# Optimization experiments

Measured on AMD Instinct MI355X. Metric: run time of the kernel, lower is better.

Reference implementation:

```python
import jax, jax.numpy as jnp
import numpy as np

B, K, R = 16, 256, 256          # batch, text length, encoder dim (r_out_size)
CONV_OUT = 8                    # l_conv_out_size
SW_C = 16                       # l_swish_c_out_size
SW_W = 16                       # l_swish_w_out_size
KS = 3                          # l_conv_kernel_size
T_MAX = 1000                    # torch.clamp(pred_mel_len, max=1000) -> static frame dim
BN_EPS = 1e-5
LN_EPS = 1e-5


def _layer_norm(x, g, b):
    mu = jnp.mean(x, -1, keepdims=True)
    var = jnp.var(x, -1, keepdims=True)
    return (x - mu) * jax.lax.rsqrt(var + LN_EPS) * g + b


def _conv_block(V, w, b, bn_g, bn_b, ln_g, ln_b):
    # ConvBlock: Conv1d(SAME) -> eval BatchNorm (running mean 0 / var 1) -> SiLU -> LayerNorm
    x = jax.lax.conv_general_dilated(V, w, (1,), "SAME",
                                     dimension_numbers=("NWC", "WIO", "NWC")) + b
    x = x * (bn_g / jnp.sqrt(1.0 + BN_EPS)) + bn_b
    x = jax.nn.silu(x)
    return _layer_norm(x, ln_g, ln_b)


def _swish_block(S, E, V8, w1, b1, w2, b2):
    # SwishBlock: Linear(concat([S,E,V8], -1)) -> SiLU -> Linear -> SiLU,
    # without materializing the [B,T,K,CONV_OUT+2] concat (split the first matmul).
    base = V8 @ w1[2:] + b1                                           # [B,K,H]
    h = jax.nn.silu(S[..., None] * w1[0] + E[..., None] * w1[1] + base[:, None])  # [B,T,K,H]
    return jax.nn.silu(h @ w2 + b2)


def setup_inputs():
    key = jax.random.key(0)
    ks = jax.random.split(key, 20)
    f32 = jnp.float32

    inp = {}
    # durations ~ U[0,10): per-utterance sum ~1280 >> T_MAX, so every length clamps to T_MAX
    inp["dur"] = jax.random.uniform(ks[0], (B, K), dtype=f32) * 10.0
    inp["V"] = jax.random.normal(ks[1], (B, K, R), dtype=f32)
    inp["pos_text"] = jnp.tile(jnp.arange(K, dtype=jnp.int32)[None], (B, 1))
    inp["text_mask"] = jnp.zeros((B, K), dtype=bool)

    def n(k, shape, s):
        return jax.random.normal(k, shape, dtype=f32) * s

    for tag, i in (("c", 2), ("w", 6)):
        inp[f"conv_{tag}_w"] = n(ks[i], (KS, R, CONV_OUT), 0.05)
        inp[f"conv_{tag}_b"] = jnp.zeros((CONV_OUT,), f32)
        inp[f"bn_{tag}_g"] = jnp.ones((CONV_OUT,), f32)
        inp[f"bn_{tag}_b"] = jnp.zeros((CONV_OUT,), f32)
        inp[f"ln_{tag}_g"] = jnp.ones((CONV_OUT,), f32)
        inp[f"ln_{tag}_b"] = jnp.zeros((CONV_OUT,), f32)
    inp["swc_w1"] = n(ks[10], (CONV_OUT + 2, SW_C), 0.3)
    inp["swc_b1"] = jnp.zeros((SW_C,), f32)
    inp["swc_w2"] = n(ks[11], (SW_C, SW_C), 0.3)
    inp["swc_b2"] = jnp.zeros((SW_C,), f32)
    inp["sww_w1"] = n(ks[12], (CONV_OUT + 2, SW_W), 0.3)
    inp["sww_b1"] = jnp.zeros((SW_W,), f32)
    inp["sww_w2"] = n(ks[13], (SW_W, SW_W), 0.3)
    inp["sww_b2"] = jnp.zeros((SW_W,), f32)
    inp["proj_w_w"] = n(ks[14], (SW_W, 1), 0.3)
    inp["proj_w_b"] = jnp.zeros((1,), f32)
    inp["lin_e_w"] = n(ks[15], (SW_C, R), 0.1)
    inp["lin_e_b"] = jnp.zeros((R,), f32)
    inp["ln_o_g"] = jnp.ones((R,), f32)
    inp["ln_o_b"] = jnp.zeros((R,), f32)
    return inp


def reference(dur, V, pos_text, text_mask,
              conv_c_w, conv_c_b, bn_c_g, bn_c_b, ln_c_g, ln_c_b,
              conv_w_w, conv_w_b, bn_w_g, bn_w_b, ln_w_g, ln_w_b,
              swc_w1, swc_b1, swc_w2, swc_b2,
              sww_w1, sww_b1, sww_w2, sww_b2,
              proj_w_w, proj_w_b, lin_e_w, lin_e_b, ln_o_g, ln_o_b):
    pred_mel_len = jnp.minimum(jnp.round(dur.sum(-1)), T_MAX).astype(jnp.int32)  # [B]
    pred_mel_mask = jnp.arange(T_MAX, dtype=jnp.int32)[None, :] >= pred_mel_len[:, None]  # [B,T]
    tm = text_mask[:, None, :]       # [B,1,K]
    mm = pred_mel_mask[:, :, None]   # [B,T,1]
    attn_mask = tm | mm              # [B,T,K]

    e_k = jnp.cumsum(dur, axis=1)    # token end boundaries   [B,K]
    s_k = e_k - dur                  # token start boundaries [B,K]
    t = jnp.arange(1, T_MAX + 1, dtype=dur.dtype)[None, :, None]   # frame index [1,T,1]
    S = jnp.where(attn_mask, 0.0, t - s_k[:, None, :])             # [B,T,K]
    E = jnp.where(attn_mask, 0.0, e_k[:, None, :] - t)             # [B,T,K]

    Vw = _conv_block(V, conv_w_w, conv_w_b, bn_w_g, bn_w_b, ln_w_g, ln_w_b)
    Wh = _swish_block(S, E, Vw, sww_w1, sww_b1, sww_w2, sww_b2)    # [B,T,K,SW_W]
    logits = jnp.squeeze(Wh @ proj_w_w, -1) + proj_w_b[0]          # [B,T,K]
    logits = jnp.where(tm, -jnp.inf, logits)
    W = jax.nn.softmax(logits, axis=2)
    W = jnp.where(mm, 0.0, W)

    Vc = _conv_block(V, conv_c_w, conv_c_b, bn_c_g, bn_c_b, ln_c_g, ln_c_b)
    C = _swish_block(S, E, Vc, swc_w1, swc_b1, swc_w2, swc_b2)     # [B,T,K,SW_C]

    agg = jnp.einsum("btk,btkp->btp", W, C)                        # [B,T,SW_C]
    up = jnp.matmul(W, V) + (agg @ lin_e_w + lin_e_b)              # [B,T,R]
    up = _layer_norm(up, ln_o_g, ln_o_b)
    up = jnp.where(pred_mel_mask[..., None], 0.0, up)
    return up, pred_mel_mask, pred_mel_len, W
```

## Files before the change

kernel.cpp:

```cpp
#include <hip/hip_runtime.h>
#include <cstddef>

constexpr int Bn = 16, Kn = 256, Rn = 256, Tn = 1000, C8 = 8, SW = 16;
constexpr size_t UP_SZ    = (size_t)Bn * Tn * Rn;
constexpr size_t MASK_OFF = UP_SZ;
constexpr size_t LEN_OFF  = MASK_OFF + (size_t)Bn * Tn;
constexpr size_t W_OFF    = LEN_OFF + Bn;

using half4_t = __attribute__((ext_vector_type(4))) _Float16;
using f32x4_t = __attribute__((ext_vector_type(4))) float;
using uint2_t = __attribute__((ext_vector_type(2))) unsigned int;

__device__ __forceinline__ float fast_rcp(float x) { return __builtin_amdgcn_rcpf(x); }
__device__ __forceinline__ float fast_exp2(float x) { return __builtin_amdgcn_exp2f(x); }
constexpr float LOG2E = 1.44269504088896340736f;
__device__ __forceinline__ float silu_f(float x) {
    return x * fast_rcp(1.f + fast_exp2(-LOG2E * x));
}

__device__ __forceinline__ void split4(const float x0, const float x1,
                                       const float x2, const float x3,
                                       half4_t& hi, half4_t& lo)
{
    const auto h01 = __builtin_amdgcn_cvt_pkrtz(x0, x1);
    const auto h23 = __builtin_amdgcn_cvt_pkrtz(x2, x3);
    uint2_t uh; uh.x = __builtin_bit_cast(unsigned int, h01);
    uh.y = __builtin_bit_cast(unsigned int, h23);
    hi = __builtin_bit_cast(half4_t, uh);
    const auto l01 = __builtin_amdgcn_cvt_pkrtz(x0 - (float)h01.x, x1 - (float)h01.y);
    const auto l23 = __builtin_amdgcn_cvt_pkrtz(x2 - (float)h23.x, x3 - (float)h23.y);
    uint2_t ul; ul.x = __builtin_bit_cast(unsigned int, l01);
    ul.y = __builtin_bit_cast(unsigned int, l23);
    lo = __builtin_bit_cast(half4_t, ul);
}

__global__ __launch_bounds__(256) void conv_partial_kernel(
    const float* __restrict__ V,
    const float* __restrict__ wW, const float* __restrict__ wC,
    float* __restrict__ part)
{
    const int rc = blockIdx.x, b = blockIdx.y, k = threadIdx.x;
    constexpr int RPAD = 33;
    __shared__ float vt[258 * RPAD];
    if (k < 16) {
        const int row = (k < 8) ? 0 : 257;
        const int j = (k & 7) * 4;
        vt[row * RPAD + j] = 0.f; vt[row * RPAD + j + 1] = 0.f;
        vt[row * RPAD + j + 2] = 0.f; vt[row * RPAD + j + 3] = 0.f;
    }
    const float* vsrc = V + ((size_t)(b * Kn + k)) * Rn + rc * 32;
#pragma unroll
    for (int j = 0; j < 8; j++) {
        const float4 qv = *(const float4*)(vsrc + j * 4);
        float* dst = &vt[(k + 1) * RPAD + j * 4];
        dst[0] = qv.x; dst[1] = qv.y; dst[2] = qv.z; dst[3] = qv.w;
    }
    __syncthreads();

    float aw[C8], ac[C8];
#pragma unroll
    for (int c = 0; c < C8; c++) { aw[c] = 0.f; ac[c] = 0.f; }
    for (int dk = 0; dk < 3; dk++) {
        const float* wp = wW + (size_t)(dk * Rn + rc * 32) * C8;
        const float* cp = wC + (size_t)(dk * Rn + rc * 32) * C8;
        const float* vrow = &vt[(k + dk) * RPAD];
#pragma unroll 4
        for (int r = 0; r < 32; r++) {
            const float v = vrow[r];
#pragma unroll
            for (int c = 0; c < C8; c++) {
                aw[c] = fmaf(v, wp[r * C8 + c], aw[c]);
                ac[c] = fmaf(v, cp[r * C8 + c], ac[c]);
            }
        }
    }
    float* dst = part + ((size_t)(b * 8 + rc) * Kn + k) * 16;
    *(float4*)(dst + 0)  = make_float4(aw[0], aw[1], aw[2], aw[3]);
    *(float4*)(dst + 4)  = make_float4(aw[4], aw[5], aw[6], aw[7]);
    *(float4*)(dst + 8)  = make_float4(ac[0], ac[1], ac[2], ac[3]);
    *(float4*)(dst + 12) = make_float4(ac[4], ac[5], ac[6], ac[7]);
}

__device__ __forceinline__ void conv_post(
    const float* acc, const float* cb, const float* bng, const float* bnb,
    const float* lng, const float* lnb, const float* w1, const float* b1,
    float* __restrict__ dst)
{
    const float bnscale = rsqrtf(1.f + 1e-5f);
    float x[C8];
    float mu = 0.f;
#pragma unroll
    for (int c = 0; c < C8; c++) {
        float v = (acc[c] + cb[c]) * (bng[c] * bnscale) + bnb[c];
        v = silu_f(v);
        x[c] = v; mu += v;
    }
    mu *= (1.f / C8);
    float var = 0.f;
#pragma unroll
    for (int c = 0; c < C8; c++) { float dd = x[c] - mu; var += dd * dd; }
    var *= (1.f / C8);
    const float rs = rsqrtf(var + 1e-5f);
    float y[C8];
#pragma unroll
    for (int c = 0; c < C8; c++) y[c] = (x[c] - mu) * rs * lng[c] + lnb[c];
#pragma unroll
    for (int c2 = 0; c2 < SW; c2++) {
        float a = b1[c2];
#pragma unroll
        for (int p = 0; p < C8; p++) a = fmaf(y[p], w1[(2 + p) * SW + c2], a);
        dst[c2] = a;
    }
}

__global__ __launch_bounds__(256) void conv_scan_finish_kernel(
    const float* __restrict__ dur,
    const float* __restrict__ part,
    const unsigned char* __restrict__ tmask_g,
    const float* __restrict__ bW, const float* __restrict__ bngW, const float* __restrict__ bnbW,
    const float* __restrict__ lngW, const float* __restrict__ lnbW,
    const float* __restrict__ bC, const float* __restrict__ bngC, const float* __restrict__ bnbC,
    const float* __restrict__ lngC, const float* __restrict__ lnbC,
    const float* __restrict__ sww_w1, const float* __restrict__ sww_b1,
    const float* __restrict__ swc_w1, const float* __restrict__ swc_b1,
    float* __restrict__ alpha_ws, float* __restrict__ ab_ws,
    int* __restrict__ len_ws, float* __restrict__ out)
{
    const int b = blockIdx.x, k = threadIdx.x;
    __shared__ float sc[Kn];
    const float d = dur[b * Kn + k];
    sc[k] = d;
    __syncthreads();
    for (int off = 1; off < Kn; off <<= 1) {
        float v = (k >= off) ? sc[k - off] : 0.f;
        __syncthreads();
        sc[k] += v;
        __syncthreads();
    }
    const float ek = sc[k];
    const float sk = ek - d;
    const float total = sc[Kn - 1];
    int len = (int)rintf(total);
    if (len > Tn) len = Tn;
    if (k == 0) { len_ws[b] = len; out[LEN_OFF + b] = (float)len; }
    for (int t = k; t < Tn; t += 256)
        out[MASK_OFF + (size_t)b * Tn + t] = (t >= len) ? 1.f : 0.f;
    if (b == 0 && k < 16) {
        alpha_ws[k]      = sww_w1[k] - sww_w1[SW + k];
        alpha_ws[16 + k] = swc_w1[k] - swc_w1[SW + k];
    }

    float aw[C8], ac[C8];
#pragma unroll
    for (int c = 0; c < C8; c++) { aw[c] = 0.f; ac[c] = 0.f; }
#pragma unroll 2
    for (int rc = 0; rc < 8; rc++) {
        const float4* p = (const float4*)(part + ((size_t)(b * 8 + rc) * Kn + k) * 16);
        const float4 q0 = p[0], q1 = p[1], q2 = p[2], q3 = p[3];
        aw[0] += q0.x; aw[1] += q0.y; aw[2] += q0.z; aw[3] += q0.w;
        aw[4] += q1.x; aw[5] += q1.y; aw[6] += q1.z; aw[7] += q1.w;
        ac[0] += q2.x; ac[1] += q2.y; ac[2] += q2.z; ac[3] += q2.w;
        ac[4] += q3.x; ac[5] += q3.y; ac[6] += q3.z; ac[7] += q3.w;
    }
    float basew[SW], basec[SW];
    conv_post(aw, bW, bngW, bnbW, lngW, lnbW, sww_w1, sww_b1, basew);
    conv_post(ac, bC, bngC, bnbC, lngC, lnbC, swc_w1, swc_b1, basec);

    const bool msk = tmask_g[b * Kn + k] != 0;
    float* dst = ab_ws + ((size_t)(b * Kn) + k) * 32;
#pragma unroll
    for (int c = 0; c < SW; c++) {
        const float w0w = sww_w1[c], w1w_ = sww_w1[SW + c];
        const float w0c = swc_w1[c], w1c_ = swc_w1[SW + c];
        dst[c]      = msk ? basew[c] : fmaf(ek, w1w_, fmaf(-sk, w0w, basew[c]));
        dst[16 + c] = msk ? basec[c] : fmaf(ek, w1c_, fmaf(-sk, w0c, basec[c]));
    }
}

__global__ __launch_bounds__(256) void logits_kernel(
    const unsigned char* __restrict__ tm, const int* __restrict__ len_ws,
    const float* __restrict__ alpha_ws, const float* __restrict__ ab_ws,
    const float* __restrict__ sww_w2, const float* __restrict__ sww_b2,
    const float* __restrict__ proj_w, const float* __restrict__ proj_b,
    const float* __restrict__ swc_w2, const float* __restrict__ swc_b2,
    float* __restrict__ agg_ws, float* __restrict__ out)
{
    const int t0 = blockIdx.x * 4, b = blockIdx.y, tid = threadIdx.x;
    const int lane = tid & 63, w = tid >> 6, q = lane >> 4, m = lane & 15;
    const int len = len_ws[b];

    __shared__ __align__(16) unsigned int hA[256 * 10];
    __shared__ __align__(16) unsigned int hB[256 * 10];
    __shared__ __align__(16) unsigned int hC[256 * 10];
    __shared__ float red[8];
    __shared__ __align__(16) float aggw[2][4][16];

    float bw[16], bc[16];
    {
        const float4* bp = (const float4*)(ab_ws + (((size_t)b * Kn) + tid) * 32);
#pragma unroll
        for (int i = 0; i < 4; i++) {
            const float4 v = bp[i];
            bw[4*i] = v.x; bw[4*i+1] = v.y; bw[4*i+2] = v.z; bw[4*i+3] = v.w;
        }
#pragma unroll
        for (int i = 0; i < 4; i++) {
            const float4 v = bp[4 + i];
            bc[4*i] = v.x; bc[4*i+1] = v.y; bc[4*i+2] = v.z; bc[4*i+3] = v.w;
        }
    }
    const float mk = (tm[b * Kn + tid] != 0) ? 0.f : 1.f;

    half4_t AWhi, AWlo, ACf;
    float pj[4], b2wv[4], b2cv[4], mb[4];
#pragma unroll
    for (int i = 0; i < 4; i++) {
        const int c = 4 * q + i;
        const float vw = sww_w2[c * SW + m];
        const _Float16 hi = (_Float16)vw;
        AWhi[i] = hi;
        AWlo[i] = (_Float16)(vw - (float)hi);
        ACf[i]  = (_Float16)(swc_w2[c * SW + m]);
        pj[i]   = proj_w[c];
        b2wv[i] = sww_b2[c];
        b2cv[i] = swc_b2[c];
        mb[i]   = (tm[b * Kn + 64 * w + 16 * i + m] != 0) ? -INFINITY : 0.f;
    }
    const float pb = proj_b[0];

    int pend = -1, pendpar = 0;

    for (int ti = 0; ti < 4; ti++) {
        const int t = t0 + ti;
        float* __restrict__ W_out = out + W_OFF + ((size_t)b * Tn + t) * Kn;
        if (t >= len) { W_out[tid] = 0.f; continue; }
        const float u = (float)(t + 1);
        const float umk = u * mk;

#pragma unroll
        for (int p = 0; p < 8; p++) {
            const float x0 = fmaf(umk, alpha_ws[2*p],   bw[2*p]);
            const float x1 = fmaf(umk, alpha_ws[2*p+1], bw[2*p+1]);
            const float h0 = silu_f(x0), h1 = silu_f(x1);
            const auto hp = __builtin_amdgcn_cvt_pkrtz(h0, h1);
            hA[tid * 10 + p] = __builtin_bit_cast(unsigned int, hp);
            const float l0 = h0 - (float)hp.x, l1 = h1 - (float)hp.y;
            hB[tid * 10 + p] = __builtin_bit_cast(unsigned int,
                                __builtin_amdgcn_cvt_pkrtz(l0, l1));
            const float y0 = fmaf(umk, alpha_ws[16 + 2*p],   bc[2*p]);
            const float y1 = fmaf(umk, alpha_ws[16 + 2*p+1], bc[2*p+1]);
            hC[tid * 10 + p] = __builtin_bit_cast(unsigned int,
                                __builtin_amdgcn_cvt_pkrtz(silu_f(y0), silu_f(y1)));
        }

        f32x4_t o[4];
#pragma unroll
        for (int j = 0; j < 4; j++) {
            const int row = 64 * w + 16 * j + m;
            const uint2_t rh = *(const uint2_t*)&hA[row * 10 + 2 * q];
            const uint2_t rl = *(const uint2_t*)&hB[row * 10 + 2 * q];
            const half4_t bh = __builtin_bit_cast(half4_t, rh);
            const half4_t bl = __builtin_bit_cast(half4_t, rl);
            f32x4_t acc = {0.f, 0.f, 0.f, 0.f};
            acc = __builtin_amdgcn_mfma_f32_16x16x16f16(AWlo, bh, acc, 0, 0, 0);
            acc = __builtin_amdgcn_mfma_f32_16x16x16f16(AWhi, bl, acc, 0, 0, 0);
            acc = __builtin_amdgcn_mfma_f32_16x16x16f16(AWhi, bh, acc, 0, 0, 0);
            o[j] = acc;
        }

        float lg[4];
#pragma unroll
        for (int j = 0; j < 4; j++) {
            float s = silu_f(o[j][0] + b2wv[0]) * pj[0];
            s = fmaf(silu_f(o[j][1] + b2wv[1]), pj[1], s);
            s = fmaf(silu_f(o[j][2] + b2wv[2]), pj[2], s);
            s = fmaf(silu_f(o[j][3] + b2wv[3]), pj[3], s);
            s += __shfl_xor(s, 16, 64);
            s += __shfl_xor(s, 32, 64);
            lg[j] = s + pb + mb[j];
        }

        float mx = fmaxf(fmaxf(lg[0], lg[1]), fmaxf(lg[2], lg[3]));
#pragma unroll
        for (int off = 1; off <= 8; off <<= 1) mx = fmaxf(mx, __shfl_xor(mx, off, 64));
        if (lane == 0) red[w] = mx;
        __syncthreads();
        if (pend >= 0) {
            if (tid < 16)
                agg_ws[((size_t)b * Tn + pend) * 16 + tid] =
                    aggw[pendpar][0][tid] + aggw[pendpar][1][tid] +
                    aggw[pendpar][2][tid] + aggw[pendpar][3][tid];
            pend = -1;
        }
        const float M = fmaxf(fmaxf(red[0], red[1]), fmaxf(red[2], red[3]));
        float pex[4];
#pragma unroll
        for (int j = 0; j < 4; j++) pex[j] = fast_exp2(LOG2E * (lg[j] - M));
        float ssum = (pex[0] + pex[1]) + (pex[2] + pex[3]);
#pragma unroll
        for (int off = 1; off <= 8; off <<= 1) ssum += __shfl_xor(ssum, off, 64);
        if (lane == 0) red[4 + w] = ssum;
        __syncthreads();
        const float inv = fast_rcp(red[4] + red[5] + red[6] + red[7]);
        float wgt[4];
#pragma unroll
        for (int j = 0; j < 4; j++) wgt[j] = pex[j] * inv;
        if (q == 0) {
#pragma unroll
            for (int j = 0; j < 4; j++) W_out[64 * w + 16 * j + m] = wgt[j];
        }

        f32x4_t ap = {0.f, 0.f, 0.f, 0.f};
#pragma unroll
        for (int j = 0; j < 4; j++) {
            const int row = 64 * w + 16 * j + m;
            const uint2_t rc2 = *(const uint2_t*)&hC[row * 10 + 2 * q];
            f32x4_t zz = {0.f, 0.f, 0.f, 0.f};
            const f32x4_t oc = __builtin_amdgcn_mfma_f32_16x16x16f16(
                ACf, __builtin_bit_cast(half4_t, rc2), zz, 0, 0, 0);
#pragma unroll
            for (int i = 0; i < 4; i++)
                ap[i] = fmaf(silu_f(oc[i] + b2cv[i]), wgt[j], ap[i]);
        }
#pragma unroll
        for (int off = 1; off <= 8; off <<= 1) {
            ap[0] += __shfl_xor(ap[0], off, 64);
            ap[1] += __shfl_xor(ap[1], off, 64);
            ap[2] += __shfl_xor(ap[2], off, 64);
            ap[3] += __shfl_xor(ap[3], off, 64);
        }
        if (m == 0)
            *(float4*)&aggw[ti & 1][w][4 * q] = make_float4(ap[0], ap[1], ap[2], ap[3]);
        pend = t; pendpar = ti & 1;
    }
    if (pend >= 0) {
        __syncthreads();
        if (tid < 16)
            agg_ws[((size_t)b * Tn + pend) * 16 + tid] =
                aggw[pendpar][0][tid] + aggw[pendpar][1][tid] +
                aggw[pendpar][2][tid] + aggw[pendpar][3][tid];
    }
}

__global__ __launch_bounds__(256) void matvec_mfma_kernel(
    const float* __restrict__ Wg, const float* __restrict__ V,
    float* __restrict__ out)
{
    const int tb = blockIdx.x, rq = blockIdx.y, b = blockIdx.z;
    const int t0 = tb * 32, r0 = rq * 64;
    const int tid = threadIdx.x;
    const int lane = tid & 63, w = tid >> 6, q = lane >> 4, m = lane & 15;
    __shared__ float4 Wl[32 * 64];

    const float4* Wg4 = (const float4*)Wg;
#pragma unroll
    for (int ch = 0; ch < 8; ch++) {
        const int idx = ch * 256 + tid;
        const int row = idx >> 6, sl = idx & 63;
        const int t = t0 + row;
        const float4 v = (t < Tn) ? Wg4[((size_t)b * Tn + t) * 64 + sl]
                                  : make_float4(0.f, 0.f, 0.f, 0.f);
        Wl[row * 64 + (sl ^ (row & 7))] = v;
    }
    __syncthreads();

    const int tt = w & 1;
    const int rp = w >> 1;
    const int wrow = tt * 16 + m;
    const int rcol = r0 + rp * 32 + m;
    const float* Vb = V + (size_t)b * Kn * Rn;

    f32x4_t acc0 = {0.f, 0.f, 0.f, 0.f};
    f32x4_t acc1 = {0.f, 0.f, 0.f, 0.f};

#pragma unroll
    for (int ks = 0; ks < 16; ks++) {
        const float4 wv = Wl[wrow * 64 + ((ks * 4 + q) ^ (wrow & 7))];
        half4_t Ahi, Alo;
        split4(wv.x, wv.y, wv.z, wv.w, Ahi, Alo);

        const float* vp = Vb + (size_t)(ks * 16 + 4 * q) * Rn;
        const float b00 = vp[rcol],          b01 = vp[Rn + rcol];
        const float b02 = vp[2 * Rn + rcol], b03 = vp[3 * Rn + rcol];
        const float b10 = vp[rcol + 16],          b11 = vp[Rn + rcol + 16];
        const float b12 = vp[2 * Rn + rcol + 16], b13 = vp[3 * Rn + rcol + 16];
        half4_t Bh0, Bl0, Bh1, Bl1;
        split4(b00, b01, b02, b03, Bh0, Bl0);
        split4(b10, b11, b12, b13, Bh1, Bl1);

        acc0 = __builtin_amdgcn_mfma_f32_16x16x16f16(Alo, Bh0, acc0, 0, 0, 0);
        acc0 = __builtin_amdgcn_mfma_f32_16x16x16f16(Ahi, Bl0, acc0, 0, 0, 0);
        acc0 = __builtin_amdgcn_mfma_f32_16x16x16f16(Ahi, Bh0, acc0, 0, 0, 0);
        acc1 = __builtin_amdgcn_mfma_f32_16x16x16f16(Alo, Bh1, acc1, 0, 0, 0);
        acc1 = __builtin_amdgcn_mfma_f32_16x16x16f16(Ahi, Bl1, acc1, 0, 0, 0);
        acc1 = __builtin_amdgcn_mfma_f32_16x16x16f16(Ahi, Bh1, acc1, 0, 0, 0);
    }

#pragma unroll
    for (int i = 0; i < 4; i++) {
        const int t = t0 + tt * 16 + 4 * q + i;
        if (t < Tn) {
            float* rowp = out + ((size_t)b * Tn + t) * Rn + rcol;
            rowp[0]  = acc0[i];
            rowp[16] = acc1[i];
        }
    }
}

__global__ __launch_bounds__(256) void ln_kernel(
    const float* __restrict__ agg_ws, const int* __restrict__ len_ws,
    const float* __restrict__ lin_e_w, const float* __restrict__ lin_e_b,
    const float* __restrict__ ln_o_g, const float* __restrict__ ln_o_b,
    float* __restrict__ out)
{
    const int b = blockIdx.y, tid = threadIdx.x;
    const int sub = tid >> 6, lane = tid & 63;
    const int t = blockIdx.x * 4 + sub;
    const int r0 = lane * 4;
    float* __restrict__ row = out + ((size_t)b * Tn + t) * Rn;
    const int len = len_ws[b];
    if (t >= len) {
        *(float4*)(row + r0) = make_float4(0.f, 0.f, 0.f, 0.f);
        return;
    }

    float4 acc = *(const float4*)(row + r0);
    {
        const float4 be = *(const float4*)(lin_e_b + r0);
        acc.x += be.x; acc.y += be.y; acc.z += be.z; acc.w += be.w;
    }
    const float* aggp = agg_ws + ((size_t)b * Tn + t) * 16;
#pragma unroll
    for (int p = 0; p < 16; p++) {
        const float a = aggp[p];
        const float4 l = *(const float4*)(lin_e_w + p * Rn + r0);
        acc.x = fmaf(a, l.x, acc.x); acc.y = fmaf(a, l.y, acc.y);
        acc.z = fmaf(a, l.z, acc.z); acc.w = fmaf(a, l.w, acc.w);
    }

    float s = (acc.x + acc.y) + (acc.z + acc.w);
#pragma unroll
    for (int off = 1; off <= 32; off <<= 1) s += __shfl_xor(s, off, 64);
    const float mu = s * (1.f / Rn);
    const float d0 = acc.x - mu, d1 = acc.y - mu, d2 = acc.z - mu, d3 = acc.w - mu;
    float vr = d0 * d0 + d1 * d1 + d2 * d2 + d3 * d3;
#pragma unroll
    for (int off = 1; off <= 32; off <<= 1) vr += __shfl_xor(vr, off, 64);
    const float rs = rsqrtf(vr * (1.f / Rn) + 1e-5f);

    const float4 g = *(const float4*)(ln_o_g + r0);
    const float4 bb = *(const float4*)(ln_o_b + r0);
    float4 res;
    res.x = d0 * rs * g.x + bb.x;
    res.y = d1 * rs * g.y + bb.y;
    res.z = d2 * rs * g.z + bb.z;
    res.w = d3 * rs * g.w + bb.w;
    *(float4*)(row + r0) = res;
}

extern "C" void kernel_launch(void* const* d_in, const int* in_sizes, int n_in,
                              void* d_out, int out_size, void* d_ws, size_t ws_size,
                              hipStream_t stream)
{
    const float* dur       = (const float*)d_in[0];
    const float* V         = (const float*)d_in[1];
    const unsigned char* text_mask = (const unsigned char*)d_in[3];
    const float* conv_c_w  = (const float*)d_in[4];
    const float* conv_c_b  = (const float*)d_in[5];
    const float* bn_c_g    = (const float*)d_in[6];
    const float* bn_c_b    = (const float*)d_in[7];
    const float* ln_c_g    = (const float*)d_in[8];
    const float* ln_c_b    = (const float*)d_in[9];
    const float* conv_w_w  = (const float*)d_in[10];
    const float* conv_w_b  = (const float*)d_in[11];
    const float* bn_w_g    = (const float*)d_in[12];
    const float* bn_w_b    = (const float*)d_in[13];
    const float* ln_w_g    = (const float*)d_in[14];
    const float* ln_w_b    = (const float*)d_in[15];
    const float* swc_w1    = (const float*)d_in[16];
    const float* swc_b1    = (const float*)d_in[17];
    const float* swc_w2    = (const float*)d_in[18];
    const float* swc_b2    = (const float*)d_in[19];
    const float* sww_w1    = (const float*)d_in[20];
    const float* sww_b1    = (const float*)d_in[21];
    const float* sww_w2    = (const float*)d_in[22];
    const float* sww_b2    = (const float*)d_in[23];
    const float* proj_w_w  = (const float*)d_in[24];
    const float* proj_w_b  = (const float*)d_in[25];
    const float* lin_e_w   = (const float*)d_in[26];
    const float* lin_e_b   = (const float*)d_in[27];
    const float* ln_o_g    = (const float*)d_in[28];
    const float* ln_o_b    = (const float*)d_in[29];

    float* out = (float*)d_out;
    float* wsf = (float*)d_ws;
    int*   len_ws   = (int*)wsf;
    float* alpha_ws = wsf + 64;
    float* ab_ws    = wsf + 128;
    float* scratch  = ab_ws + 131072;
    float* part     = scratch;
    float* agg_ws   = scratch;

    conv_partial_kernel<<<dim3(8, Bn), dim3(256), 0, stream>>>(V, conv_w_w, conv_c_w, part);
    conv_scan_finish_kernel<<<dim3(Bn), dim3(256), 0, stream>>>(
        dur, part, text_mask,
        conv_w_b, bn_w_g, bn_w_b, ln_w_g, ln_w_b,
        conv_c_b, bn_c_g, bn_c_b, ln_c_g, ln_c_b,
        sww_w1, sww_b1, swc_w1, swc_b1,
        alpha_ws, ab_ws, len_ws, out);
    logits_kernel<<<dim3(Tn / 4, Bn), dim3(256), 0, stream>>>(
        text_mask, len_ws, alpha_ws, ab_ws,
        sww_w2, sww_b2, proj_w_w, proj_w_b,
        swc_w2, swc_b2,
        agg_ws, out);
    matvec_mfma_kernel<<<dim3((Tn + 31) / 32, 4, Bn), dim3(256), 0, stream>>>(
        out + W_OFF, V, out);
    ln_kernel<<<dim3(Tn / 4, Bn), dim3(256), 0, stream>>>(
        agg_ws, len_ws, lin_e_w, lin_e_b, ln_o_g, ln_o_b, out);
}
```

Measured before the change: 160.5 us.

## Fuse logits, W·V matvec and output layernorm into one kernel

```diff
diff --git a/kernel.cpp b/kernel.cpp
--- a/kernel.cpp
+++ b/kernel.cpp
@@ -177,23 +177,28 @@
     }
 }
 
-__global__ __launch_bounds__(256) void logits_kernel(
+__global__ __launch_bounds__(256) void fused_kernel(
     const unsigned char* __restrict__ tm, const int* __restrict__ len_ws,
     const float* __restrict__ alpha_ws, const float* __restrict__ ab_ws,
     const float* __restrict__ sww_w2, const float* __restrict__ sww_b2,
     const float* __restrict__ proj_w, const float* __restrict__ proj_b,
     const float* __restrict__ swc_w2, const float* __restrict__ swc_b2,
-    float* __restrict__ agg_ws, float* __restrict__ out)
-{
-    const int t0 = blockIdx.x * 4, b = blockIdx.y, tid = threadIdx.x;
+    const float* __restrict__ V,
+    const float* __restrict__ lin_e_w, const float* __restrict__ lin_e_b,
+    const float* __restrict__ ln_o_g, const float* __restrict__ ln_o_b,
+    float* __restrict__ out)
+{
+    const int t0 = blockIdx.x * 16, b = blockIdx.y, tid = threadIdx.x;
     const int lane = tid & 63, w = tid >> 6, q = lane >> 4, m = lane & 15;
     const int len = len_ws[b];
 
-    __shared__ __align__(16) unsigned int hA[256 * 10];
-    __shared__ __align__(16) unsigned int hB[256 * 10];
-    __shared__ __align__(16) unsigned int hC[256 * 10];
+    __shared__ __align__(16) unsigned int POOL[7680];
+    __shared__ __align__(16) float Wl[16 * 256];
+    __shared__ __align__(16) float aggp[16][4][16];
     __shared__ float red[8];
-    __shared__ __align__(16) float aggw[2][4][16];
+    unsigned int* hA = POOL;
+    unsigned int* hB = POOL + 2560;
+    unsigned int* hC = POOL + 5120;
 
     float bw[16], bc[16];
     {
@@ -228,12 +233,13 @@
     }
     const float pb = proj_b[0];
 
-    int pend = -1, pendpar = 0;
-
-    for (int ti = 0; ti < 4; ti++) {
+    for (int ti = 0; ti < 16; ti++) {
         const int t = t0 + ti;
-        float* __restrict__ W_out = out + W_OFF + ((size_t)b * Tn + t) * Kn;
-        if (t >= len) { W_out[tid] = 0.f; continue; }
+        if (t >= len) {
+            if (t < Tn) out[W_OFF + ((size_t)b * Tn + t) * Kn + tid] = 0.f;
+            Wl[ti * 256 + (((tid >> 2) ^ (ti & 7)) << 2) + (tid & 3)] = 0.f;
+            continue;
+        }
         const float u = (float)(t + 1);
         const float umk = u * mk;
 
@@ -285,13 +291,6 @@
         for (int off = 1; off <= 8; off <<= 1) mx = fmaxf(mx, __shfl_xor(mx, off, 64));
         if (lane == 0) red[w] = mx;
         __syncthreads();
-        if (pend >= 0) {
-            if (tid < 16)
-                agg_ws[((size_t)b * Tn + pend) * 16 + tid] =
-                    aggw[pendpar][0][tid] + aggw[pendpar][1][tid] +
-                    aggw[pendpar][2][tid] + aggw[pendpar][3][tid];
-            pend = -1;
-        }
         const float M = fmaxf(fmaxf(red[0], red[1]), fmaxf(red[2], red[3]));
         float pex[4];
 #pragma unroll
@@ -306,8 +305,13 @@
 #pragma unroll
         for (int j = 0; j < 4; j++) wgt[j] = pex[j] * inv;
         if (q == 0) {
-#pragma unroll
-            for (int j = 0; j < 4; j++) W_out[64 * w + 16 * j + m] = wgt[j];
+            float* __restrict__ W_out = out + W_OFF + ((size_t)b * Tn + t) * Kn;
+#pragma unroll
+            for (int j = 0; j < 4; j++) {
+                const int k = 64 * w + 16 * j + m;
+                W_out[k] = wgt[j];
+                Wl[ti * 256 + ((((k >> 2)) ^ (ti & 7)) << 2) + (k & 3)] = wgt[j];
+            }
         }
 
         f32x4_t ap = {0.f, 0.f, 0.f, 0.f};
@@ -330,132 +334,83 @@
             ap[3] += __shfl_xor(ap[3], off, 64);
         }
         if (m == 0)
-            *(float4*)&aggw[ti & 1][w][4 * q] = make_float4(ap[0], ap[1], ap[2], ap[3]);
-        pend = t; pendpar = ti & 1;
-    }
-    if (pend >= 0) {
-        __syncthreads();
-        if (tid < 16)
-            agg_ws[((size_t)b * Tn + pend) * 16 + tid] =
-                aggw[pendpar][0][tid] + aggw[pendpar][1][tid] +
-                aggw[pendpar][2][tid] + aggw[pendpar][3][tid];
-    }
-}
-
-__global__ __launch_bounds__(256) void matvec_mfma_kernel(
-    const float* __restrict__ Wg, const float* __restrict__ V,
-    float* __restrict__ out)
-{
-    const int tb = blockIdx.x, rq = blockIdx.y, b = blockIdx.z;
-    const int t0 = tb * 32, r0 = rq * 64;
-    const int tid = threadIdx.x;
-    const int lane = tid & 63, w = tid >> 6, q = lane >> 4, m = lane & 15;
-    __shared__ float4 Wl[32 * 64];
-
-    const float4* Wg4 = (const float4*)Wg;
-#pragma unroll
-    for (int ch = 0; ch < 8; ch++) {
-        const int idx = ch * 256 + tid;
-        const int row = idx >> 6, sl = idx & 63;
-        const int t = t0 + row;
-        const float4 v = (t < Tn) ? Wg4[((size_t)b * Tn + t) * 64 + sl]
-                                  : make_float4(0.f, 0.f, 0.f, 0.f);
-        Wl[row * 64 + (sl ^ (row & 7))] = v;
+            *(float4*)&aggp[ti][w][4 * q] = make_float4(ap[0], ap[1], ap[2], ap[3]);
     }
     __syncthreads();
 
-    const int tt = w & 1;
-    const int rp = w >> 1;
-    const int wrow = tt * 16 + m;
-    const int rcol = r0 + rp * 32 + m;
+    f32x4_t acc[4];
+#pragma unroll
+    for (int i = 0; i < 4; i++) acc[i] = f32x4_t{0.f, 0.f, 0.f, 0.f};
     const float* Vb = V + (size_t)b * Kn * Rn;
 
-    f32x4_t acc0 = {0.f, 0.f, 0.f, 0.f};
-    f32x4_t acc1 = {0.f, 0.f, 0.f, 0.f};
-
 #pragma unroll
     for (int ks = 0; ks < 16; ks++) {
-        const float4 wv = Wl[wrow * 64 + ((ks * 4 + q) ^ (wrow & 7))];
+        const float4 wv = *(const float4*)&Wl[m * 256 + (((4 * ks + q) ^ (m & 7)) << 2)];
         half4_t Ahi, Alo;
         split4(wv.x, wv.y, wv.z, wv.w, Ahi, Alo);
-
         const float* vp = Vb + (size_t)(ks * 16 + 4 * q) * Rn;
-        const float b00 = vp[rcol],          b01 = vp[Rn + rcol];
-        const float b02 = vp[2 * Rn + rcol], b03 = vp[3 * Rn + rcol];
-        const float b10 = vp[rcol + 16],          b11 = vp[Rn + rcol + 16];
-        const float b12 = vp[2 * Rn + rcol + 16], b13 = vp[3 * Rn + rcol + 16];
-        half4_t Bh0, Bl0, Bh1, Bl1;
-        split4(b00, b01, b02, b03, Bh0, Bl0);
-        split4(b10, b11, b12, b13, Bh1, Bl1);
-
-        acc0 = __builtin_amdgcn_mfma_f32_16x16x16f16(Alo, Bh0, acc0, 0, 0, 0);
-        acc0 = __builtin_amdgcn_mfma_f32_16x16x16f16(Ahi, Bl0, acc0, 0, 0, 0);
-        acc0 = __builtin_amdgcn_mfma_f32_16x16x16f16(Ahi, Bh0, acc0, 0, 0, 0);
-        acc1 = __builtin_amdgcn_mfma_f32_16x16x16f16(Alo, Bh1, acc1, 0, 0, 0);
-        acc1 = __builtin_amdgcn_mfma_f32_16x16x16f16(Ahi, Bl1, acc1, 0, 0, 0);
-        acc1 = __builtin_amdgcn_mfma_f32_16x16x16f16(Ahi, Bh1, acc1, 0, 0, 0);
-    }
-
-#pragma unroll
-    for (int i = 0; i < 4; i++) {
-        const int t = t0 + tt * 16 + 4 * q + i;
-        if (t < Tn) {
-            float* rowp = out + ((size_t)b * Tn + t) * Rn + rcol;
-            rowp[0]  = acc0[i];
-            rowp[16] = acc1[i];
-        }
-    }
-}
-
-__global__ __launch_bounds__(256) void ln_kernel(
-    const float* __restrict__ agg_ws, const int* __restrict__ len_ws,
-    const float* __restrict__ lin_e_w, const float* __restrict__ lin_e_b,
-    const float* __restrict__ ln_o_g, const float* __restrict__ ln_o_b,
-    float* __restrict__ out)
-{
-    const int b = blockIdx.y, tid = threadIdx.x;
-    const int sub = tid >> 6, lane = tid & 63;
-    const int t = blockIdx.x * 4 + sub;
-    const int r0 = lane * 4;
-    float* __restrict__ row = out + ((size_t)b * Tn + t) * Rn;
-    const int len = len_ws[b];
-    if (t >= len) {
-        *(float4*)(row + r0) = make_float4(0.f, 0.f, 0.f, 0.f);
-        return;
-    }
-
-    float4 acc = *(const float4*)(row + r0);
-    {
-        const float4 be = *(const float4*)(lin_e_b + r0);
-        acc.x += be.x; acc.y += be.y; acc.z += be.z; acc.w += be.w;
-    }
-    const float* aggp = agg_ws + ((size_t)b * Tn + t) * 16;
-#pragma unroll
-    for (int p = 0; p < 16; p++) {
-        const float a = aggp[p];
-        const float4 l = *(const float4*)(lin_e_w + p * Rn + r0);
-        acc.x = fmaf(a, l.x, acc.x); acc.y = fmaf(a, l.y, acc.y);
-        acc.z = fmaf(a, l.z, acc.z); acc.w = fmaf(a, l.w, acc.w);
-    }
-
-    float s = (acc.x + acc.y) + (acc.z + acc.w);
-#pragma unroll
-    for (int off = 1; off <= 32; off <<= 1) s += __shfl_xor(s, off, 64);
-    const float mu = s * (1.f / Rn);
-    const float d0 = acc.x - mu, d1 = acc.y - mu, d2 = acc.z - mu, d3 = acc.w - mu;
-    float vr = d0 * d0 + d1 * d1 + d2 * d2 + d3 * d3;
-#pragma unroll
-    for (int off = 1; off <= 32; off <<= 1) vr += __shfl_xor(vr, off, 64);
-    const float rs = rsqrtf(vr * (1.f / Rn) + 1e-5f);
-
-    const float4 g = *(const float4*)(ln_o_g + r0);
-    const float4 bb = *(const float4*)(ln_o_b + r0);
-    float4 res;
-    res.x = d0 * rs * g.x + bb.x;
-    res.y = d1 * rs * g.y + bb.y;
-    res.z = d2 * rs * g.z + bb.z;
-    res.w = d3 * rs * g.w + bb.w;
-    *(float4*)(row + r0) = res;
+#pragma unroll
+        for (int rt = 0; rt < 4; rt++) {
+            const int rcol = w * 64 + rt * 16 + m;
+            const float b0 = vp[rcol],          b1 = vp[Rn + rcol];
+            const float b2 = vp[2 * Rn + rcol], b3 = vp[3 * Rn + rcol];
+            half4_t Bh, Bl;
+            split4(b0, b1, b2, b3, Bh, Bl);
+            acc[rt] = __builtin_amdgcn_mfma_f32_16x16x16f16(Alo, Bh, acc[rt], 0, 0, 0);
+            acc[rt] = __builtin_amdgcn_mfma_f32_16x16x16f16(Ahi, Bl, acc[rt], 0, 0, 0);
+            acc[rt] = __builtin_amdgcn_mfma_f32_16x16x16f16(Ahi, Bh, acc[rt], 0, 0, 0);
+        }
+    }
+    float* raw = (float*)POOL;
+#pragma unroll
+    for (int rt = 0; rt < 4; rt++) {
+#pragma unroll
+        for (int i = 0; i < 4; i++)
+            raw[(4 * q + i) * 260 + w * 64 + rt * 16 + m] = acc[rt][i];
+    }
+    __syncthreads();
+
+#pragma unroll
+    for (int j = 0; j < 4; j++) {
+        const int tl = 4 * w + j;
+        const int t = t0 + tl;
+        if (t >= Tn) continue;
+        float* __restrict__ row = out + ((size_t)b * Tn + t) * Rn;
+        const int r0 = lane * 4;
+        if (t >= len) {
+            *(float4*)(row + r0) = make_float4(0.f, 0.f, 0.f, 0.f);
+            continue;
+        }
+        float4 a4 = *(const float4*)&raw[tl * 260 + r0];
+        {
+            const float4 be = *(const float4*)(lin_e_b + r0);
+            a4.x += be.x; a4.y += be.y; a4.z += be.z; a4.w += be.w;
+        }
+#pragma unroll
+        for (int p = 0; p < 16; p++) {
+            const float a = aggp[tl][0][p] + aggp[tl][1][p] + aggp[tl][2][p] + aggp[tl][3][p];
+            const float4 l = *(const float4*)(lin_e_w + p * Rn + r0);
+            a4.x = fmaf(a, l.x, a4.x); a4.y = fmaf(a, l.y, a4.y);
+            a4.z = fmaf(a, l.z, a4.z); a4.w = fmaf(a, l.w, a4.w);
+        }
+        float s = (a4.x + a4.y) + (a4.z + a4.w);
+#pragma unroll
+        for (int off = 1; off <= 32; off <<= 1) s += __shfl_xor(s, off, 64);
+        const float mu = s * (1.f / Rn);
+        const float d0 = a4.x - mu, d1 = a4.y - mu, d2 = a4.z - mu, d3 = a4.w - mu;
+        float vr = d0 * d0 + d1 * d1 + d2 * d2 + d3 * d3;
+#pragma unroll
+        for (int off = 1; off <= 32; off <<= 1) vr += __shfl_xor(vr, off, 64);
+        const float rs = rsqrtf(vr * (1.f / Rn) + 1e-5f);
+        const float4 g = *(const float4*)(ln_o_g + r0);
+        const float4 bb = *(const float4*)(ln_o_b + r0);
+        float4 res;
+        res.x = d0 * rs * g.x + bb.x;
+        res.y = d1 * rs * g.y + bb.y;
+        res.z = d2 * rs * g.z + bb.z;
+        res.w = d3 * rs * g.w + bb.w;
+        *(float4*)(row + r0) = res;
+    }
 }
 
 extern "C" void kernel_launch(void* const* d_in, const int* in_sizes, int n_in,
@@ -497,9 +452,7 @@
     int*   len_ws   = (int*)wsf;
     float* alpha_ws = wsf + 64;
     float* ab_ws    = wsf + 128;
-    float* scratch  = ab_ws + 131072;
-    float* part     = scratch;
-    float* agg_ws   = scratch;
+    float* part     = ab_ws + 131072;
 
     conv_partial_kernel<<<dim3(8, Bn), dim3(256), 0, stream>>>(V, conv_w_w, conv_c_w, part);
     conv_scan_finish_kernel<<<dim3(Bn), dim3(256), 0, stream>>>(
@@ -508,13 +461,9 @@
         conv_c_b, bn_c_g, bn_c_b, ln_c_g, ln_c_b,
         sww_w1, sww_b1, swc_w1, swc_b1,
         alpha_ws, ab_ws, len_ws, out);
-    logits_kernel<<<dim3(Tn / 4, Bn), dim3(256), 0, stream>>>(
+    fused_kernel<<<dim3((Tn + 15) / 16, Bn), dim3(256), 0, stream>>>(
         text_mask, len_ws, alpha_ws, ab_ws,
         sww_w2, sww_b2, proj_w_w, proj_w_b,
         swc_w2, swc_b2,
-        agg_ws, out);
-    matvec_mfma_kernel<<<dim3((Tn + 31) / 32, 4, Bn), dim3(256), 0, stream>>>(
-        out + W_OFF, V, out);
-    ln_kernel<<<dim3(Tn / 4, Bn), dim3(256), 0, stream>>>(
-        agg_ws, len_ws, lin_e_w, lin_e_b, ln_o_g, ln_o_b, out);
-}
+        V, lin_e_w, lin_e_b, ln_o_g, ln_o_b, out);
+}
```

Result: slower. 164.8 us (+2.7%).

## Give each wavefront its own frame in logits kernel, dropping block syncs

Applied to the files above, without the earlier changes.

```diff
diff --git a/kernel.cpp b/kernel.cpp
--- a/kernel.cpp
+++ b/kernel.cpp
@@ -167,13 +167,13 @@
     conv_post(ac, bC, bngC, bnbC, lngC, lnbC, swc_w1, swc_b1, basec);
 
     const bool msk = tmask_g[b * Kn + k] != 0;
-    float* dst = ab_ws + ((size_t)(b * Kn) + k) * 32;
+    float* dstb = ab_ws + (size_t)b * 8192;
 #pragma unroll
     for (int c = 0; c < SW; c++) {
         const float w0w = sww_w1[c], w1w_ = sww_w1[SW + c];
         const float w0c = swc_w1[c], w1c_ = swc_w1[SW + c];
-        dst[c]      = msk ? basew[c] : fmaf(ek, w1w_, fmaf(-sk, w0w, basew[c]));
-        dst[16 + c] = msk ? basec[c] : fmaf(ek, w1c_, fmaf(-sk, w0c, basec[c]));
+        dstb[c * 256 + k]        = msk ? basew[c] : fmaf(ek, w1w_, fmaf(-sk, w0w, basew[c]));
+        dstb[(16 + c) * 256 + k] = msk ? basec[c] : fmaf(ek, w1c_, fmaf(-sk, w0c, basec[c]));
     }
 }
 
@@ -185,142 +185,156 @@
     const float* __restrict__ swc_w2, const float* __restrict__ swc_b2,
     float* __restrict__ agg_ws, float* __restrict__ out)
 {
-    const int t0 = blockIdx.x * 4, b = blockIdx.y, tid = threadIdx.x;
+    const int t0 = blockIdx.x * 16, b = blockIdx.y, tid = threadIdx.x;
     const int lane = tid & 63, w = tid >> 6, q = lane >> 4, m = lane & 15;
     const int len = len_ws[b];
 
-    __shared__ __align__(16) unsigned int hA[256 * 10];
-    __shared__ __align__(16) unsigned int hB[256 * 10];
-    __shared__ __align__(16) unsigned int hC[256 * 10];
-    __shared__ float red[8];
-    __shared__ __align__(16) float aggw[2][4][16];
-
-    float bw[16], bc[16];
-    {
-        const float4* bp = (const float4*)(ab_ws + (((size_t)b * Kn) + tid) * 32);
-#pragma unroll
-        for (int i = 0; i < 4; i++) {
-            const float4 v = bp[i];
-            bw[4*i] = v.x; bw[4*i+1] = v.y; bw[4*i+2] = v.z; bw[4*i+3] = v.w;
-        }
-#pragma unroll
-        for (int i = 0; i < 4; i++) {
-            const float4 v = bp[4 + i];
-            bc[4*i] = v.x; bc[4*i+1] = v.y; bc[4*i+2] = v.z; bc[4*i+3] = v.w;
-        }
-    }
-    const float mk = (tm[b * Kn + tid] != 0) ? 0.f : 1.f;
+    __shared__ __align__(16) unsigned int BUF[4][2][648];
+    unsigned int* hi_buf = &BUF[w][0][0];
+    unsigned int* lo_buf = &BUF[w][1][0];
 
     half4_t AWhi, AWlo, ACf;
-    float pj[4], b2wv[4], b2cv[4], mb[4];
+    float pj[4], b2wv[4], b2cv[4];
 #pragma unroll
     for (int i = 0; i < 4; i++) {
         const int c = 4 * q + i;
         const float vw = sww_w2[c * SW + m];
-        const _Float16 hi = (_Float16)vw;
-        AWhi[i] = hi;
-        AWlo[i] = (_Float16)(vw - (float)hi);
+        const _Float16 hif = (_Float16)vw;
+        AWhi[i] = hif;
+        AWlo[i] = (_Float16)(vw - (float)hif);
         ACf[i]  = (_Float16)(swc_w2[c * SW + m]);
         pj[i]   = proj_w[c];
         b2wv[i] = sww_b2[c];
         b2cv[i] = swc_b2[c];
-        mb[i]   = (tm[b * Kn + 64 * w + 16 * i + m] != 0) ? -INFINITY : 0.f;
     }
     const float pb = proj_b[0];
 
-    int pend = -1, pendpar = 0;
-
-    for (int ti = 0; ti < 4; ti++) {
-        const int t = t0 + ti;
+    float aW[16], aC[16];
+#pragma unroll
+    for (int c = 0; c < 16; c++) { aW[c] = alpha_ws[c]; aC[c] = alpha_ws[16 + c]; }
+    float mbv[16];
+#pragma unroll
+    for (int j = 0; j < 16; j++)
+        mbv[j] = (tm[b * Kn + 16 * j + m] != 0) ? -INFINITY : 0.f;
+    float mk4[4];
+#pragma unroll
+    for (int g = 0; g < 4; g++)
+        mk4[g] = (tm[b * Kn + 64 * g + lane] != 0) ? 0.f : 1.f;
+
+    const float* abW = ab_ws + (size_t)b * 8192;
+    const float* abC = abW + 4096;
+
+    for (int s = 0; s < 4; s++) {
+        const int t = t0 + 4 * w + s;
+        if (t >= len) {
+            if (t < Tn) {
+                float* __restrict__ W_out = out + W_OFF + ((size_t)b * Tn + t) * Kn;
+#pragma unroll
+                for (int jj = 0; jj < 4; jj++)
+                    W_out[16 * (4 * q + jj) + m] = 0.f;
+            }
+            continue;
+        }
         float* __restrict__ W_out = out + W_OFF + ((size_t)b * Tn + t) * Kn;
-        if (t >= len) { W_out[tid] = 0.f; continue; }
         const float u = (float)(t + 1);
-        const float umk = u * mk;
-
-#pragma unroll
-        for (int p = 0; p < 8; p++) {
-            const float x0 = fmaf(umk, alpha_ws[2*p],   bw[2*p]);
-            const float x1 = fmaf(umk, alpha_ws[2*p+1], bw[2*p+1]);
-            const float h0 = silu_f(x0), h1 = silu_f(x1);
-            const auto hp = __builtin_amdgcn_cvt_pkrtz(h0, h1);
-            hA[tid * 10 + p] = __builtin_bit_cast(unsigned int, hp);
-            const float l0 = h0 - (float)hp.x, l1 = h1 - (float)hp.y;
-            hB[tid * 10 + p] = __builtin_bit_cast(unsigned int,
-                                __builtin_amdgcn_cvt_pkrtz(l0, l1));
-            const float y0 = fmaf(umk, alpha_ws[16 + 2*p],   bc[2*p]);
-            const float y1 = fmaf(umk, alpha_ws[16 + 2*p+1], bc[2*p+1]);
-            hC[tid * 10 + p] = __builtin_bit_cast(unsigned int,
-                                __builtin_amdgcn_cvt_pkrtz(silu_f(y0), silu_f(y1)));
-        }
-
-        f32x4_t o[4];
-#pragma unroll
-        for (int j = 0; j < 4; j++) {
-            const int row = 64 * w + 16 * j + m;
-            const uint2_t rh = *(const uint2_t*)&hA[row * 10 + 2 * q];
-            const uint2_t rl = *(const uint2_t*)&hB[row * 10 + 2 * q];
-            const half4_t bh = __builtin_bit_cast(half4_t, rh);
-            const half4_t bl = __builtin_bit_cast(half4_t, rl);
-            f32x4_t acc = {0.f, 0.f, 0.f, 0.f};
-            acc = __builtin_amdgcn_mfma_f32_16x16x16f16(AWlo, bh, acc, 0, 0, 0);
-            acc = __builtin_amdgcn_mfma_f32_16x16x16f16(AWhi, bl, acc, 0, 0, 0);
-            acc = __builtin_amdgcn_mfma_f32_16x16x16f16(AWhi, bh, acc, 0, 0, 0);
-            o[j] = acc;
-        }
-
-        float lg[4];
-#pragma unroll
-        for (int j = 0; j < 4; j++) {
-            float s = silu_f(o[j][0] + b2wv[0]) * pj[0];
-            s = fmaf(silu_f(o[j][1] + b2wv[1]), pj[1], s);
-            s = fmaf(silu_f(o[j][2] + b2wv[2]), pj[2], s);
-            s = fmaf(silu_f(o[j][3] + b2wv[3]), pj[3], s);
-            s += __shfl_xor(s, 16, 64);
-            s += __shfl_xor(s, 32, 64);
-            lg[j] = s + pb + mb[j];
-        }
-
-        float mx = fmaxf(fmaxf(lg[0], lg[1]), fmaxf(lg[2], lg[3]));
-#pragma unroll
-        for (int off = 1; off <= 8; off <<= 1) mx = fmaxf(mx, __shfl_xor(mx, off, 64));
-        if (lane == 0) red[w] = mx;
-        __syncthreads();
-        if (pend >= 0) {
-            if (tid < 16)
-                agg_ws[((size_t)b * Tn + pend) * 16 + tid] =
-                    aggw[pendpar][0][tid] + aggw[pendpar][1][tid] +
-                    aggw[pendpar][2][tid] + aggw[pendpar][3][tid];
-            pend = -1;
-        }
-        const float M = fmaxf(fmaxf(red[0], red[1]), fmaxf(red[2], red[3]));
-        float pex[4];
-#pragma unroll
-        for (int j = 0; j < 4; j++) pex[j] = fast_exp2(LOG2E * (lg[j] - M));
-        float ssum = (pex[0] + pex[1]) + (pex[2] + pex[3]);
+
+        float lg[16];
+#pragma unroll
+        for (int g = 0; g < 4; g++) {
+            const int k = 64 * g + lane;
+            const float umk = u * mk4[g];
+            unsigned int hp8[8], lp8[8];
+#pragma unroll
+            for (int p = 0; p < 8; p++) {
+                const float x0 = fmaf(umk, aW[2 * p],     abW[(2 * p) * 256 + k]);
+                const float x1 = fmaf(umk, aW[2 * p + 1], abW[(2 * p + 1) * 256 + k]);
+                const float h0 = silu_f(x0), h1 = silu_f(x1);
+                const auto hp = __builtin_amdgcn_cvt_pkrtz(h0, h1);
+                hp8[p] = __builtin_bit_cast(unsigned int, hp);
+                lp8[p] = __builtin_bit_cast(unsigned int,
+                          __builtin_amdgcn_cvt_pkrtz(h0 - (float)hp.x, h1 - (float)hp.y));
+            }
+#pragma unroll
+            for (int p = 0; p < 4; p++) {
+                uint2_t a; a.x = hp8[2 * p]; a.y = hp8[2 * p + 1];
+                *(uint2_t*)&hi_buf[lane * 10 + 2 * p] = a;
+                uint2_t bb; bb.x = lp8[2 * p]; bb.y = lp8[2 * p + 1];
+                *(uint2_t*)&lo_buf[lane * 10 + 2 * p] = bb;
+            }
+#pragma unroll
+            for (int jj = 0; jj < 4; jj++) {
+                const int row = 16 * jj + m;
+                const half4_t bh = __builtin_bit_cast(half4_t, *(const uint2_t*)&hi_buf[row * 10 + 2 * q]);
+                const half4_t bl = __builtin_bit_cast(half4_t, *(const uint2_t*)&lo_buf[row * 10 + 2 * q]);
+                f32x4_t o = {0.f, 0.f, 0.f, 0.f};
+                o = __builtin_amdgcn_mfma_f32_16x16x16f16(AWlo, bh, o, 0, 0, 0);
+                o = __builtin_amdgcn_mfma_f32_16x16x16f16(AWhi, bl, o, 0, 0, 0);
+                o = __builtin_amdgcn_mfma_f32_16x16x16f16(AWhi, bh, o, 0, 0, 0);
+                float ss = silu_f(o[0] + b2wv[0]) * pj[0];
+                ss = fmaf(silu_f(o[1] + b2wv[1]), pj[1], ss);
+                ss = fmaf(silu_f(o[2] + b2wv[2]), pj[2], ss);
+                ss = fmaf(silu_f(o[3] + b2wv[3]), pj[3], ss);
+                ss += __shfl_xor(ss, 16, 64);
+                ss += __shfl_xor(ss, 32, 64);
+                lg[4 * g + jj] = ss + pb + mbv[4 * g + jj];
+            }
+        }
+
+        float M = lg[0];
+#pragma unroll
+        for (int j = 1; j < 16; j++) M = fmaxf(M, lg[j]);
+#pragma unroll
+        for (int off = 1; off <= 8; off <<= 1) M = fmaxf(M, __shfl_xor(M, off, 64));
+        float wgt[16];
+        float ssum = 0.f;
+#pragma unroll
+        for (int j = 0; j < 16; j++) {
+            wgt[j] = fast_exp2(LOG2E * (lg[j] - M));
+            ssum += wgt[j];
+        }
 #pragma unroll
         for (int off = 1; off <= 8; off <<= 1) ssum += __shfl_xor(ssum, off, 64);
-        if (lane == 0) red[4 + w] = ssum;
-        __syncthreads();
-        const float inv = fast_rcp(red[4] + red[5] + red[6] + red[7]);
-        float wgt[4];
-#pragma unroll
-        for (int j = 0; j < 4; j++) wgt[j] = pex[j] * inv;
-        if (q == 0) {
-#pragma unroll
-            for (int j = 0; j < 4; j++) W_out[64 * w + 16 * j + m] = wgt[j];
+        const float inv = fast_rcp(ssum);
+#pragma unroll
+        for (int j = 0; j < 16; j++) wgt[j] *= inv;
+
+#pragma unroll
+        for (int jj = 0; jj < 4; jj++) {
+            float v = wgt[jj];
+            v = (q == 1) ? wgt[4 + jj]  : v;
+            v = (q == 2) ? wgt[8 + jj]  : v;
+            v = (q == 3) ? wgt[12 + jj] : v;
+            W_out[16 * (4 * q + jj) + m] = v;
         }
 
         f32x4_t ap = {0.f, 0.f, 0.f, 0.f};
 #pragma unroll
-        for (int j = 0; j < 4; j++) {
-            const int row = 64 * w + 16 * j + m;
-            const uint2_t rc2 = *(const uint2_t*)&hC[row * 10 + 2 * q];
-            f32x4_t zz = {0.f, 0.f, 0.f, 0.f};
-            const f32x4_t oc = __builtin_amdgcn_mfma_f32_16x16x16f16(
-                ACf, __builtin_bit_cast(half4_t, rc2), zz, 0, 0, 0);
-#pragma unroll
-            for (int i = 0; i < 4; i++)
-                ap[i] = fmaf(silu_f(oc[i] + b2cv[i]), wgt[j], ap[i]);
+        for (int g = 0; g < 4; g++) {
+            const int k = 64 * g + lane;
+            const float umk = u * mk4[g];
+            unsigned int cp8[8];
+#pragma unroll
+            for (int p = 0; p < 8; p++) {
+                const float y0 = fmaf(umk, aC[2 * p],     abC[(2 * p) * 256 + k]);
+                const float y1 = fmaf(umk, aC[2 * p + 1], abC[(2 * p + 1) * 256 + k]);
+                cp8[p] = __builtin_bit_cast(unsigned int,
+                          __builtin_amdgcn_cvt_pkrtz(silu_f(y0), silu_f(y1)));
+            }
+#pragma unroll
+            for (int p = 0; p < 4; p++) {
+                uint2_t a; a.x = cp8[2 * p]; a.y = cp8[2 * p + 1];
+                *(uint2_t*)&hi_buf[lane * 10 + 2 * p] = a;
+            }
+#pragma unroll
+            for (int jj = 0; jj < 4; jj++) {
+                const int row = 16 * jj + m;
+                const half4_t bc = __builtin_bit_cast(half4_t, *(const uint2_t*)&hi_buf[row * 10 + 2 * q]);
+                f32x4_t zz = {0.f, 0.f, 0.f, 0.f};
+                const f32x4_t oc = __builtin_amdgcn_mfma_f32_16x16x16f16(ACf, bc, zz, 0, 0, 0);
+#pragma unroll
+                for (int i = 0; i < 4; i++)
+                    ap[i] = fmaf(silu_f(oc[i] + b2cv[i]), wgt[4 * g + jj], ap[i]);
+            }
         }
 #pragma unroll
         for (int off = 1; off <= 8; off <<= 1) {
@@ -330,15 +344,8 @@
             ap[3] += __shfl_xor(ap[3], off, 64);
         }
         if (m == 0)
-            *(float4*)&aggw[ti & 1][w][4 * q] = make_float4(ap[0], ap[1], ap[2], ap[3]);
-        pend = t; pendpar = ti & 1;
-    }
-    if (pend >= 0) {
-        __syncthreads();
-        if (tid < 16)
-            agg_ws[((size_t)b * Tn + pend) * 16 + tid] =
-                aggw[pendpar][0][tid] + aggw[pendpar][1][tid] +
-                aggw[pendpar][2][tid] + aggw[pendpar][3][tid];
+            *(float4*)&agg_ws[((size_t)b * Tn + t) * 16 + 4 * q] =
+                make_float4(ap[0], ap[1], ap[2], ap[3]);
     }
 }
 
@@ -508,7 +515,7 @@
         conv_c_b, bn_c_g, bn_c_b, ln_c_g, ln_c_b,
         sww_w1, sww_b1, swc_w1, swc_b1,
         alpha_ws, ab_ws, len_ws, out);
-    logits_kernel<<<dim3(Tn / 4, Bn), dim3(256), 0, stream>>>(
+    logits_kernel<<<dim3((Tn + 15) / 16, Bn), dim3(256), 0, stream>>>(
         text_mask, len_ws, alpha_ws, ab_ws,
         sww_w2, sww_b2, proj_w_w, proj_w_b,
         swc_w2, swc_b2,
```

Result: slower. 356.9 us (+122.4%).
